# Performance work log

Hardware: AMD Instinct MI355X
Metric: run time of the kernel (lower is better)

Reference implementation:

```python
import jax, jax.numpy as jnp
import numpy as np

N_NODES = 50000
N_EDGES = 400000
D = 128


def _rgg_layer(x, src, tgt, Wk, Wq, Wv, Ws, b, n_nodes):
    # Node-level projections (dense GEMMs, as in PyG which applies Linear before message passing)
    k = x @ Wk  # lin_key, gathered at targets
    q = x @ Wq  # lin_query, gathered at sources
    v = x @ Wv  # lin_value, gathered at sources
    # Per-edge gather + sigmoid gate + elementwise message
    eta = jax.nn.sigmoid(k[tgt] + q[src])  # [E, D]
    msg = eta * v[src]                      # [E, D]
    # Scatter-add aggregation to target nodes
    agg = jax.ops.segment_sum(msg, tgt, num_segments=n_nodes)
    # Root/skip connection + bias
    return agg + x @ Ws + b


def setup_inputs() -> dict:
    key = jax.random.key(0)
    ks = jax.random.split(key, 12)
    s = 1.0 / np.sqrt(D)
    x = jax.random.normal(ks[0], (N_NODES, D), dtype=jnp.float32)
    edge_index = jax.random.randint(ks[1], (2, N_EDGES), 0, N_NODES, dtype=jnp.int64)
    W = lambda k: (jax.random.normal(k, (D, D), dtype=jnp.float32) * s)
    return {
        "x": x,
        "edge_index": edge_index,
        "Wk1": W(ks[2]), "Wq1": W(ks[3]), "Wv1": W(ks[4]), "Ws1": W(ks[5]),
        "b1": jnp.zeros((D,), dtype=jnp.float32),
        "Wk2": W(ks[6]), "Wq2": W(ks[7]), "Wv2": W(ks[8]), "Ws2": W(ks[9]),
        "b2": jnp.zeros((D,), dtype=jnp.float32),
    }


def reference(x, edge_index, Wk1, Wq1, Wv1, Ws1, b1, Wk2, Wq2, Wv2, Ws2, b2):
    src, tgt = edge_index[0], edge_index[1]
    n = x.shape[0]
    h = _rgg_layer(x, src, tgt, Wk1, Wq1, Wv1, Ws1, b1, n)
    h = jax.nn.relu(h)
    # F.dropout treated as identity (deterministic/inference reference)
    out = _rgg_layer(h, src, tgt, Wk2, Wq2, Wv2, Ws2, b2, n)
    return out
```

## Files before the change

### kernel.cpp

```cpp
#include <hip/hip_runtime.h>

#define N_NODES 50000
#define D 128
#define N_EDGES 400000
#define NCHUNKS ((N_NODES + 255) / 256)
#define NBLK ((N_NODES + 127) / 128)
#define W_FRAG_SHORTS 16384

typedef short s8v  __attribute__((ext_vector_type(8)));
typedef float f4v  __attribute__((ext_vector_type(4)));

__device__ __forceinline__ unsigned short f2bf(float f) {
    unsigned int u = __float_as_uint(f);
    u += 0x7FFFu + ((u >> 16) & 1u);
    return (unsigned short)(u >> 16);
}
__device__ __forceinline__ float bflo(unsigned int u) { return __uint_as_float(u << 16); }
__device__ __forceinline__ float bfhi(unsigned int u) { return __uint_as_float(u & 0xFFFF0000u); }
__device__ __forceinline__ float sigm(float x) {
    return __builtin_amdgcn_rcpf(1.f + __expf(-x));
}

__global__ __launch_bounds__(256)
void cvt_bf16(const float* __restrict__ X, short* __restrict__ Xb)
{
    const size_t i = ((size_t)blockIdx.x * 256 + threadIdx.x) * 8;
    float4 a0 = *(const float4*)(X + i);
    float4 a1 = *(const float4*)(X + i + 4);
    s8v v;
    v[0] = (short)f2bf(a0.x); v[1] = (short)f2bf(a0.y);
    v[2] = (short)f2bf(a0.z); v[3] = (short)f2bf(a0.w);
    v[4] = (short)f2bf(a1.x); v[5] = (short)f2bf(a1.y);
    v[6] = (short)f2bf(a1.z); v[7] = (short)f2bf(a1.w);
    *(s8v*)(Xb + i) = v;
}

__global__ __launch_bounds__(256)
void make_wt(const float* __restrict__ W0, const float* __restrict__ W1,
             const float* __restrict__ W2, const float* __restrict__ W3,
             const float* __restrict__ W4, const float* __restrict__ W5,
             const float* __restrict__ W6, const float* __restrict__ W7,
             short* __restrict__ Wt)
{
    const int wsel = blockIdx.x;
    const float* W = (wsel == 0) ? W0 : (wsel == 1) ? W1 : (wsel == 2) ? W2 :
                     (wsel == 3) ? W3 : (wsel == 4) ? W4 : (wsel == 5) ? W5 :
                     (wsel == 6) ? W6 : W7;
    const int slot = blockIdx.y * 256 + threadIdx.x;
    const int frag = slot >> 6;
    const int lane = slot & 63;
    const int n    = (frag >> 2) * 16 + (lane & 15);
    const int kc   = frag & 3;
    const int quad = lane >> 4;
    const int k0   = kc * 32 + quad * 8;

    s8v v;
#pragma unroll
    for (int j = 0; j < 8; ++j)
        v[j] = (short)f2bf(W[(size_t)(k0 + j) * D + n]);
    *(s8v*)(Wt + (size_t)wsel * W_FRAG_SHORTS + (size_t)slot * 8) = v;
}

__global__ __launch_bounds__(256)
void gemm_mfma(const short* __restrict__ Xb, const short* __restrict__ WtL,
               const float* __restrict__ bias,
               short* __restrict__ Kb, short* __restrict__ QV,
               float* __restrict__ Agg)
{
    __shared__ short As[16384];

    const int m0  = blockIdx.x * 128;
    const int sel = blockIdx.y;
    const int tid = threadIdx.x;

#pragma unroll
    for (int i = 0; i < 8; ++i) {
        const int m   = (tid >> 4) + 16 * i;
        const int oct = tid & 15;
        const int row = m0 + m;
        s8v v = (s8v){0, 0, 0, 0, 0, 0, 0, 0};
        if (row < N_NODES)
            v = *(const s8v*)(Xb + (size_t)row * D + oct * 8);
        const int kc   = oct >> 2;
        const int quad = oct & 3;
        const int frag = (m >> 4) * 4 + kc;
        const int slot = ((m & 15) + 16 * quad) ^ (kc << 1);
        *(s8v*)&As[frag * 512 + slot * 8] = v;
    }
    __syncthreads();

    const int lane = tid & 63;
    const int w    = tid >> 6;
    const short* __restrict__ Wf = WtL + (size_t)sel * W_FRAG_SHORTS;

    f4v acc[2][8];
#pragma unroll
    for (int mt = 0; mt < 2; ++mt)
#pragma unroll
        for (int nt = 0; nt < 8; ++nt)
            acc[mt][nt] = (f4v){0.f, 0.f, 0.f, 0.f};

#pragma unroll
    for (int kc = 0; kc < 4; ++kc) {
        const int sl = (lane ^ (kc << 1)) * 8;
        s8v a0 = *(const s8v*)&As[((2 * w + 0) * 4 + kc) * 512 + sl];
        s8v a1 = *(const s8v*)&As[((2 * w + 1) * 4 + kc) * 512 + sl];
#pragma unroll
        for (int nt = 0; nt < 8; ++nt) {
            s8v b = *(const s8v*)(Wf + (size_t)(nt * 4 + kc) * 512 + lane * 8);
            acc[0][nt] = __builtin_amdgcn_mfma_f32_16x16x32_bf16(a0, b, acc[0][nt], 0, 0, 0);
            acc[1][nt] = __builtin_amdgcn_mfma_f32_16x16x32_bf16(a1, b, acc[1][nt], 0, 0, 0);
        }
    }

    const int col = lane & 15;
#pragma unroll
    for (int mt = 0; mt < 2; ++mt) {
        const int rbase = m0 + (2 * w + mt) * 16 + (lane >> 4) * 4;
        if (sel == 3) {
#pragma unroll
            for (int nt = 0; nt < 8; ++nt) {
                const float bv = bias[nt * 16 + col];
#pragma unroll
                for (int i = 0; i < 4; ++i) {
                    const int row = rbase + i;
                    if (row < N_NODES)
                        Agg[(size_t)row * D + nt * 16 + col] = acc[mt][nt][i] + bv;
                }
            }
        } else {
            short* __restrict__ Outb;
            int stride, coff;
            if (sel == 0)      { Outb = Kb; stride = 128; coff = 0;   }
            else if (sel == 1) { Outb = QV; stride = 256; coff = 0;   }
            else               { Outb = QV; stride = 256; coff = 128; }
#pragma unroll
            for (int nt = 0; nt < 8; ++nt)
#pragma unroll
                for (int i = 0; i < 4; ++i) {
                    const int row = rbase + i;
                    if (row < N_NODES)
                        Outb[(size_t)row * stride + coff + nt * 16 + col] =
                            (short)f2bf(acc[mt][nt][i]);
                }
        }
    }
}

__global__ __launch_bounds__(256)
void hist_kernel(const int* __restrict__ tgt, int* __restrict__ counts)
{
    int e = blockIdx.x * 256 + threadIdx.x;
    if (e < N_EDGES) atomicAdd(&counts[tgt[e]], 1);
}

__global__ __launch_bounds__(256)
void chunk_reduce(const int* __restrict__ counts, int* __restrict__ chunk_sum)
{
    __shared__ int s[256];
    int i = blockIdx.x * 256 + threadIdx.x;
    s[threadIdx.x] = (i < N_NODES) ? counts[i] : 0;
    __syncthreads();
    for (int d = 128; d > 0; d >>= 1) {
        if (threadIdx.x < d) s[threadIdx.x] += s[threadIdx.x + d];
        __syncthreads();
    }
    if (threadIdx.x == 0) chunk_sum[blockIdx.x] = s[0];
}

__global__ void scan_sums(const int* __restrict__ chunk_sum,
                          int* __restrict__ chunk_off, int* __restrict__ off)
{
    if (threadIdx.x == 0) {
        int run = 0;
        for (int i = 0; i < NCHUNKS; ++i) { chunk_off[i] = run; run += chunk_sum[i]; }
        off[N_NODES] = run;
    }
}

__global__ __launch_bounds__(256)
void scan_chunks(const int* __restrict__ counts, const int* __restrict__ chunk_off,
                 int* __restrict__ off, int* __restrict__ cursor)
{
    __shared__ int s[256];
    int i = blockIdx.x * 256 + threadIdx.x;
    int v = (i < N_NODES) ? counts[i] : 0;
    s[threadIdx.x] = v;
    __syncthreads();
    for (int d = 1; d < 256; d <<= 1) {
        int t = (threadIdx.x >= d) ? s[threadIdx.x - d] : 0;
        __syncthreads();
        s[threadIdx.x] += t;
        __syncthreads();
    }
    if (i < N_NODES) {
        int excl = s[threadIdx.x] - v + chunk_off[blockIdx.x];
        off[i]    = excl;
        cursor[i] = excl;
    }
}

__global__ __launch_bounds__(256)
void scatter_kernel(const int* __restrict__ src, const int* __restrict__ tgt,
                    int* __restrict__ cursor, int* __restrict__ es)
{
    int e = blockIdx.x * 256 + threadIdx.x;
    if (e < N_EDGES) {
        int pos = atomicAdd(&cursor[tgt[e]], 1);
        es[pos] = src[e];
    }
}

template<bool FIRST>
__global__ __launch_bounds__(256)
void node_agg(const int* __restrict__ off, const int* __restrict__ es,
              const short* __restrict__ K, const short* __restrict__ QV,
              const float* __restrict__ Skip, float* __restrict__ OutF,
              unsigned int* __restrict__ Hb)
{
    const int lane = threadIdx.x & 63;
    const int t    = __builtin_amdgcn_readfirstlane(blockIdx.x * 4 + (threadIdx.x >> 6));

    const unsigned int* __restrict__ K1  = (const unsigned int*)K;
    const unsigned int* __restrict__ QV1 = (const unsigned int*)QV;

    const unsigned int ku = K1[(size_t)t * 64 + lane];
    const float kx = bflo(ku), ky = bfhi(ku);

    float ax = 0.f, ay = 0.f, bx = 0.f, by = 0.f;
    const int e0 = __builtin_amdgcn_readfirstlane(off[t]);
    const int e1 = __builtin_amdgcn_readfirstlane(off[t + 1]);

    int e = e0;
    for (; e + 2 <= e1; e += 2) {
        const int s0 = __builtin_amdgcn_readfirstlane(es[e]);
        const int s1 = __builtin_amdgcn_readfirstlane(es[e + 1]);
        const unsigned int* r0 = QV1 + (size_t)s0 * 128;
        const unsigned int* r1 = QV1 + (size_t)s1 * 128;
        const unsigned int q0 = r0[lane], v0 = r0[64 + lane];
        const unsigned int q1 = r1[lane], v1 = r1[64 + lane];
        ax += bflo(v0) * sigm(kx + bflo(q0));
        ay += bfhi(v0) * sigm(ky + bfhi(q0));
        bx += bflo(v1) * sigm(kx + bflo(q1));
        by += bfhi(v1) * sigm(ky + bfhi(q1));
    }
    if (e < e1) {
        const int s0 = __builtin_amdgcn_readfirstlane(es[e]);
        const unsigned int* r0 = QV1 + (size_t)s0 * 128;
        const unsigned int q0 = r0[lane], v0 = r0[64 + lane];
        ax += bflo(v0) * sigm(kx + bflo(q0));
        ay += bfhi(v0) * sigm(ky + bfhi(q0));
    }

    const float2 sk = ((const float2*)Skip)[(size_t)t * 64 + lane];
    const float rx = sk.x + ax + bx;
    const float ry = sk.y + ay + by;

    if (FIRST) {
        const unsigned int lo = f2bf(fmaxf(rx, 0.f));
        const unsigned int hi = f2bf(fmaxf(ry, 0.f));
        Hb[(size_t)t * 64 + lane] = (hi << 16) | lo;
    } else {
        ((float2*)OutF)[(size_t)t * 64 + lane] = make_float2(rx, ry);
    }
}

extern "C" void kernel_launch(void* const* d_in, const int* in_sizes, int n_in,
                              void* d_out, int out_size, void* d_ws, size_t ws_size,
                              hipStream_t stream)
{
    const float* x   = (const float*)d_in[0];
    const int*   ei  = (const int*)d_in[1];
    const float* Wk1 = (const float*)d_in[2];
    const float* Wq1 = (const float*)d_in[3];
    const float* Wv1 = (const float*)d_in[4];
    const float* Ws1 = (const float*)d_in[5];
    const float* b1  = (const float*)d_in[6];
    const float* Wk2 = (const float*)d_in[7];
    const float* Wq2 = (const float*)d_in[8];
    const float* Wv2 = (const float*)d_in[9];
    const float* Ws2 = (const float*)d_in[10];
    const float* b2  = (const float*)d_in[11];

    const int* src = ei;
    const int* tgt = ei + N_EDGES;

    const size_t nd = (size_t)N_NODES * D;
    short* kb  = (short*)d_ws;
    short* qv  = kb + nd;
    short* xb  = qv + 2 * nd;
    short* hb  = xb + nd;
    float* agg1 = (float*)(hb + nd);
    short* wt  = (short*)(agg1 + nd);
    int* counts    = (int*)(wt + 8 * W_FRAG_SHORTS);
    int* off       = counts + N_NODES;
    int* cursor    = off + N_NODES + 1;
    int* es        = cursor + N_NODES;
    int* chunk_sum = es + N_EDGES;
    int* chunk_off = chunk_sum + NCHUNKS;
    float* out = (float*)d_out;

    const int eb = (N_EDGES + 255) / 256;
    dim3 gemm_grid(NBLK, 4);

    cvt_bf16<<<(int)(nd / (256 * 8)), 256, 0, stream>>>(x, xb);
    make_wt<<<dim3(8, 8), 256, 0, stream>>>(Wk1, Wq1, Wv1, Ws1, Wk2, Wq2, Wv2, Ws2, wt);
    hipMemsetAsync(counts, 0, N_NODES * sizeof(int), stream);
    hist_kernel   <<<eb, 256, 0, stream>>>(tgt, counts);
    chunk_reduce  <<<NCHUNKS, 256, 0, stream>>>(counts, chunk_sum);
    scan_sums     <<<1, 64, 0, stream>>>(chunk_sum, chunk_off, off);
    scan_chunks   <<<NCHUNKS, 256, 0, stream>>>(counts, chunk_off, off, cursor);
    scatter_kernel<<<eb, 256, 0, stream>>>(src, tgt, cursor, es);

    gemm_mfma<<<gemm_grid, 256, 0, stream>>>(xb, wt, b1, kb, qv, agg1);
    node_agg<true><<<N_NODES / 4, 256, 0, stream>>>(off, es, kb, qv, agg1, nullptr,
                                                    (unsigned int*)hb);

    gemm_mfma<<<gemm_grid, 256, 0, stream>>>(hb, wt + 4 * W_FRAG_SHORTS, b2,
                                             kb, qv, out);
    node_agg<false><<<N_NODES / 4, 256, 0, stream>>>(off, es, kb, qv, out, out, nullptr);
}
```

Before: 295.1 us.

## Fuse four projection GEMMs per row tile and interleave Q/V layout

The GEMM now runs all four weight matrices inside one block over a 64-row tile. The input tile is loaded once, and each weight fragment set is staged into LDS with global_load_lds. Results go through a swizzled LDS buffer so the bf16 and float stores are wide and coalesced. Q and V are interleaved per element pair so node_agg fetches both with a single 8-byte load per lane. The cost is more LDS, more barriers, and a serial loop over the four weights within each block.

Measured after the change: 275.6 us. 6.6% less time.

```diff
diff --git a/kernel.cpp b/kernel.cpp
--- a/kernel.cpp
+++ b/kernel.cpp
@@ -4,16 +4,19 @@
 #define D 128
 #define N_EDGES 400000
 #define NCHUNKS ((N_NODES + 255) / 256)
-#define NBLK ((N_NODES + 127) / 128)
+#define NBLK64 ((N_NODES + 63) / 64)
 #define W_FRAG_SHORTS 16384
 
 typedef short s8v  __attribute__((ext_vector_type(8)));
 typedef float f4v  __attribute__((ext_vector_type(4)));
 
-__device__ __forceinline__ unsigned short f2bf(float f) {
+__device__ __forceinline__ unsigned int f2bf(float f) {
     unsigned int u = __float_as_uint(f);
     u += 0x7FFFu + ((u >> 16) & 1u);
-    return (unsigned short)(u >> 16);
+    return u >> 16;
+}
+__device__ __forceinline__ unsigned int packbf(float a, float b) {
+    return (f2bf(b) << 16) | f2bf(a);
 }
 __device__ __forceinline__ float bflo(unsigned int u) { return __uint_as_float(u << 16); }
 __device__ __forceinline__ float bfhi(unsigned int u) { return __uint_as_float(u & 0xFFFF0000u); }
@@ -62,87 +65,116 @@
 }
 
 __global__ __launch_bounds__(256)
-void gemm_mfma(const short* __restrict__ Xb, const short* __restrict__ WtL,
-               const float* __restrict__ bias,
-               short* __restrict__ Kb, short* __restrict__ QV,
-               float* __restrict__ Agg)
-{
-    __shared__ short As[16384];
-
-    const int m0  = blockIdx.x * 128;
-    const int sel = blockIdx.y;
-    const int tid = threadIdx.x;
-
-#pragma unroll
-    for (int i = 0; i < 8; ++i) {
+void gemm_all(const short* __restrict__ Xb, const short* __restrict__ WtL,
+              const float* __restrict__ bias,
+              short* __restrict__ Kb, unsigned int* __restrict__ QV,
+              float* __restrict__ Agg)
+{
+    __shared__ __align__(16) short As[8192];
+    __shared__ __align__(16) short Bs[16384];
+    __shared__ __align__(16) float biasS[128];
+
+    const int tid  = threadIdx.x;
+    const int lane = tid & 63;
+    const int w    = tid >> 6;
+    const int wr   = w & 1;
+    const int wc   = w >> 1;
+    const int m0   = blockIdx.x * 64;
+
+    if (tid < 128) biasS[tid] = bias[tid];
+
+#pragma unroll
+    for (int i = 0; i < 4; ++i) {
         const int m   = (tid >> 4) + 16 * i;
         const int oct = tid & 15;
         const int row = m0 + m;
         s8v v = (s8v){0, 0, 0, 0, 0, 0, 0, 0};
-        if (row < N_NODES)
-            v = *(const s8v*)(Xb + (size_t)row * D + oct * 8);
-        const int kc   = oct >> 2;
-        const int quad = oct & 3;
+        if (row < N_NODES) v = *(const s8v*)(Xb + (size_t)row * D + oct * 8);
+        const int kc = oct >> 2, quad = oct & 3;
         const int frag = (m >> 4) * 4 + kc;
         const int slot = ((m & 15) + 16 * quad) ^ (kc << 1);
         *(s8v*)&As[frag * 512 + slot * 8] = v;
     }
-    __syncthreads();
-
-    const int lane = tid & 63;
-    const int w    = tid >> 6;
-    const short* __restrict__ Wf = WtL + (size_t)sel * W_FRAG_SHORTS;
-
-    f4v acc[2][8];
-#pragma unroll
-    for (int mt = 0; mt < 2; ++mt)
-#pragma unroll
-        for (int nt = 0; nt < 8; ++nt)
-            acc[mt][nt] = (f4v){0.f, 0.f, 0.f, 0.f};
-
-#pragma unroll
-    for (int kc = 0; kc < 4; ++kc) {
-        const int sl = (lane ^ (kc << 1)) * 8;
-        s8v a0 = *(const s8v*)&As[((2 * w + 0) * 4 + kc) * 512 + sl];
-        s8v a1 = *(const s8v*)&As[((2 * w + 1) * 4 + kc) * 512 + sl];
-#pragma unroll
-        for (int nt = 0; nt < 8; ++nt) {
-            s8v b = *(const s8v*)(Wf + (size_t)(nt * 4 + kc) * 512 + lane * 8);
-            acc[0][nt] = __builtin_amdgcn_mfma_f32_16x16x32_bf16(a0, b, acc[0][nt], 0, 0, 0);
-            acc[1][nt] = __builtin_amdgcn_mfma_f32_16x16x32_bf16(a1, b, acc[1][nt], 0, 0, 0);
+
+    float* Cs = (float*)Bs;
+
+    for (int sel = 0; sel < 4; ++sel) {
+        __syncthreads();
+
+        const short* Wf = WtL + (size_t)sel * W_FRAG_SHORTS;
+#pragma unroll
+        for (int j = 0; j < 8; ++j) {
+            const int chunk = tid + 256 * j;
+            __builtin_amdgcn_global_load_lds(
+                (const __attribute__((address_space(1))) unsigned int*)(Wf + chunk * 8),
+                (__attribute__((address_space(3))) unsigned int*)(&Bs[(chunk & ~63) * 8]),
+                16, 0, 0);
         }
-    }
-
-    const int col = lane & 15;
-#pragma unroll
-    for (int mt = 0; mt < 2; ++mt) {
-        const int rbase = m0 + (2 * w + mt) * 16 + (lane >> 4) * 4;
-        if (sel == 3) {
-#pragma unroll
-            for (int nt = 0; nt < 8; ++nt) {
-                const float bv = bias[nt * 16 + col];
+        __syncthreads();
+
+        f4v acc[2][4];
+#pragma unroll
+        for (int mt = 0; mt < 2; ++mt)
+#pragma unroll
+            for (int nt = 0; nt < 4; ++nt)
+                acc[mt][nt] = (f4v){0.f, 0.f, 0.f, 0.f};
+
+#pragma unroll
+        for (int kc = 0; kc < 4; ++kc) {
+            const int sl = (lane ^ (kc << 1)) * 8;
+            s8v a0 = *(const s8v*)&As[((2 * wr + 0) * 4 + kc) * 512 + sl];
+            s8v a1 = *(const s8v*)&As[((2 * wr + 1) * 4 + kc) * 512 + sl];
+#pragma unroll
+            for (int nt = 0; nt < 4; ++nt) {
+                s8v b = *(const s8v*)&Bs[((4 * wc + nt) * 4 + kc) * 512 + lane * 8];
+                acc[0][nt] = __builtin_amdgcn_mfma_f32_16x16x32_bf16(a0, b, acc[0][nt], 0, 0, 0);
+                acc[1][nt] = __builtin_amdgcn_mfma_f32_16x16x32_bf16(a1, b, acc[1][nt], 0, 0, 0);
+            }
+        }
+        __syncthreads();
+
+#pragma unroll
+        for (int mt = 0; mt < 2; ++mt) {
+            const int r0 = wr * 32 + mt * 16 + (lane >> 4) * 4;
+#pragma unroll
+            for (int nt = 0; nt < 4; ++nt) {
+                const int col = wc * 64 + nt * 16 + (lane & 15);
+                const int g = col >> 2, jj = col & 3;
 #pragma unroll
                 for (int i = 0; i < 4; ++i) {
-                    const int row = rbase + i;
-                    if (row < N_NODES)
-                        Agg[(size_t)row * D + nt * 16 + col] = acc[mt][nt][i] + bv;
+                    const int row = r0 + i;
+                    const int gs  = g ^ (((row >> 2) & 3) << 2);
+                    Cs[row * 128 + gs * 4 + jj] = acc[mt][nt][i];
                 }
             }
-        } else {
-            short* __restrict__ Outb;
-            int stride, coff;
-            if (sel == 0)      { Outb = Kb; stride = 128; coff = 0;   }
-            else if (sel == 1) { Outb = QV; stride = 256; coff = 0;   }
-            else               { Outb = QV; stride = 256; coff = 128; }
-#pragma unroll
-            for (int nt = 0; nt < 8; ++nt)
-#pragma unroll
-                for (int i = 0; i < 4; ++i) {
-                    const int row = rbase + i;
-                    if (row < N_NODES)
-                        Outb[(size_t)row * stride + coff + nt * 16 + col] =
-                            (short)f2bf(acc[mt][nt][i]);
+        }
+        __syncthreads();
+
+#pragma unroll
+        for (int j = 0; j < 8; ++j) {
+            const int c    = tid + 256 * j;
+            const int row  = c >> 5;
+            const int gg   = c & 31;
+            const int gs   = gg ^ (((row >> 2) & 3) << 2);
+            const f4v vv   = *(const f4v*)&Cs[row * 128 + gs * 4];
+            const int grow = m0 + row;
+            if (grow >= N_NODES) continue;
+            if (sel == 3) {
+                const float4 bv = *(const float4*)&biasS[gg * 4];
+                float4 o = make_float4(vv[0] + bv.x, vv[1] + bv.y,
+                                       vv[2] + bv.z, vv[3] + bv.w);
+                *(float4*)&Agg[(size_t)grow * D + gg * 4] = o;
+            } else {
+                const unsigned int p0 = packbf(vv[0], vv[1]);
+                const unsigned int p1 = packbf(vv[2], vv[3]);
+                if (sel == 0) {
+                    uint2* kp = (uint2*)((unsigned int*)Kb + (size_t)grow * 64 + gg * 2);
+                    *kp = make_uint2(p0, p1);
+                } else {
+                    unsigned int* rowp = QV + (size_t)grow * 128 + gg * 4 + (sel == 2 ? 1 : 0);
+                    rowp[0] = p0; rowp[2] = p1;
                 }
+            }
         }
     }
 }
@@ -214,17 +246,14 @@
 template<bool FIRST>
 __global__ __launch_bounds__(256)
 void node_agg(const int* __restrict__ off, const int* __restrict__ es,
-              const short* __restrict__ K, const short* __restrict__ QV,
+              const short* __restrict__ K, const unsigned int* __restrict__ QV,
               const float* __restrict__ Skip, float* __restrict__ OutF,
               unsigned int* __restrict__ Hb)
 {
     const int lane = threadIdx.x & 63;
     const int t    = __builtin_amdgcn_readfirstlane(blockIdx.x * 4 + (threadIdx.x >> 6));
 
-    const unsigned int* __restrict__ K1  = (const unsigned int*)K;
-    const unsigned int* __restrict__ QV1 = (const unsigned int*)QV;
-
-    const unsigned int ku = K1[(size_t)t * 64 + lane];
+    const unsigned int ku = ((const unsigned int*)K)[(size_t)t * 64 + lane];
     const float kx = bflo(ku), ky = bfhi(ku);
 
     float ax = 0.f, ay = 0.f, bx = 0.f, by = 0.f;
@@ -235,21 +264,18 @@
     for (; e + 2 <= e1; e += 2) {
         const int s0 = __builtin_amdgcn_readfirstlane(es[e]);
         const int s1 = __builtin_amdgcn_readfirstlane(es[e + 1]);
-        const unsigned int* r0 = QV1 + (size_t)s0 * 128;
-        const unsigned int* r1 = QV1 + (size_t)s1 * 128;
-        const unsigned int q0 = r0[lane], v0 = r0[64 + lane];
-        const unsigned int q1 = r1[lane], v1 = r1[64 + lane];
-        ax += bflo(v0) * sigm(kx + bflo(q0));
-        ay += bfhi(v0) * sigm(ky + bfhi(q0));
-        bx += bflo(v1) * sigm(kx + bflo(q1));
-        by += bfhi(v1) * sigm(ky + bfhi(q1));
+        const uint2 qv0 = ((const uint2*)(QV + (size_t)s0 * 128))[lane];
+        const uint2 qv1 = ((const uint2*)(QV + (size_t)s1 * 128))[lane];
+        ax += bflo(qv0.y) * sigm(kx + bflo(qv0.x));
+        ay += bfhi(qv0.y) * sigm(ky + bfhi(qv0.x));
+        bx += bflo(qv1.y) * sigm(kx + bflo(qv1.x));
+        by += bfhi(qv1.y) * sigm(ky + bfhi(qv1.x));
     }
     if (e < e1) {
         const int s0 = __builtin_amdgcn_readfirstlane(es[e]);
-        const unsigned int* r0 = QV1 + (size_t)s0 * 128;
-        const unsigned int q0 = r0[lane], v0 = r0[64 + lane];
-        ax += bflo(v0) * sigm(kx + bflo(q0));
-        ay += bfhi(v0) * sigm(ky + bfhi(q0));
+        const uint2 qv0 = ((const uint2*)(QV + (size_t)s0 * 128))[lane];
+        ax += bflo(qv0.y) * sigm(kx + bflo(qv0.x));
+        ay += bfhi(qv0.y) * sigm(ky + bfhi(qv0.x));
     }
 
     const float2 sk = ((const float2*)Skip)[(size_t)t * 64 + lane];
@@ -257,9 +283,7 @@
     const float ry = sk.y + ay + by;
 
     if (FIRST) {
-        const unsigned int lo = f2bf(fmaxf(rx, 0.f));
-        const unsigned int hi = f2bf(fmaxf(ry, 0.f));
-        Hb[(size_t)t * 64 + lane] = (hi << 16) | lo;
+        Hb[(size_t)t * 64 + lane] = packbf(fmaxf(rx, 0.f), fmaxf(ry, 0.f));
     } else {
         ((float2*)OutF)[(size_t)t * 64 + lane] = make_float2(rx, ry);
     }
@@ -301,7 +325,6 @@
     float* out = (float*)d_out;
 
     const int eb = (N_EDGES + 255) / 256;
-    dim3 gemm_grid(NBLK, 4);
 
     cvt_bf16<<<(int)(nd / (256 * 8)), 256, 0, stream>>>(x, xb);
     make_wt<<<dim3(8, 8), 256, 0, stream>>>(Wk1, Wq1, Wv1, Ws1, Wk2, Wq2, Wv2, Ws2, wt);
@@ -312,11 +335,12 @@
     scan_chunks   <<<NCHUNKS, 256, 0, stream>>>(counts, chunk_off, off, cursor);
     scatter_kernel<<<eb, 256, 0, stream>>>(src, tgt, cursor, es);
 
-    gemm_mfma<<<gemm_grid, 256, 0, stream>>>(xb, wt, b1, kb, qv, agg1);
-    node_agg<true><<<N_NODES / 4, 256, 0, stream>>>(off, es, kb, qv, agg1, nullptr,
-                                                    (unsigned int*)hb);
-
-    gemm_mfma<<<gemm_grid, 256, 0, stream>>>(hb, wt + 4 * W_FRAG_SHORTS, b2,
-                                             kb, qv, out);
-    node_agg<false><<<N_NODES / 4, 256, 0, stream>>>(off, es, kb, qv, out, out, nullptr);
-}
+    gemm_all<<<NBLK64, 256, 0, stream>>>(xb, wt, b1, kb, (unsigned int*)qv, agg1);
+    node_agg<true><<<N_NODES / 4, 256, 0, stream>>>(off, es, kb, (const unsigned int*)qv,
+                                                    agg1, nullptr, (unsigned int*)hb);
+
+    gemm_all<<<NBLK64, 256, 0, stream>>>(hb, wt + 4 * W_FRAG_SHORTS, b2,
+                                         kb, (unsigned int*)qv, out);
+    node_agg<false><<<N_NODES / 4, 256, 0, stream>>>(off, es, kb, (const unsigned int*)qv,
+                                                     out, out, nullptr);
+}
```
